# Kernel optimization log

Measured on AMD Instinct MI355X. Metric: run time of the kernel, lower is better.

## Reference

```python
import jax, jax.numpy as jnp
import numpy as np

MARGIN = 0.3
NEG_INF = jnp.float32(-1e30)


def setup_inputs() -> dict:
    key = jax.random.key(0)
    k1, k2 = jax.random.split(key)
    features = jax.random.normal(k1, (8192, 128), dtype=jnp.float32)
    labels = jax.random.randint(k2, (8192,), 0, 512)
    return {"features": features, "labels": labels}


def reference(features, labels):
    n = features.shape[0]
    # pairwise Euclidean distance, clamped like the torch code
    x2 = jnp.sum(features * features, axis=1, keepdims=True)          # [N,1]
    d2 = x2 + x2.T - 2.0 * (features @ features.T)                    # [N,N]
    dist = jnp.sqrt(jnp.clip(d2, 1e-8))

    same = labels[None, :] == labels[:, None]                          # [N,N]
    eye = jnp.eye(n, dtype=bool)
    pos_mask = same & ~eye                                             # positives, self excluded
    neg_mask = ~same

    # soft mining: softmax-weighted positive distance (weights ~ softmax(d))
    pos_logits = jnp.where(pos_mask, dist, NEG_INF)
    pw = jax.nn.softmax(pos_logits, axis=1)
    wp = jnp.sum(pw * jnp.where(pos_mask, dist, 0.0), axis=1)          # [N]

    # softmax-weighted negative distance (weights ~ softmax(-d))
    neg_logits = jnp.where(neg_mask, -dist, NEG_INF)
    nw = jax.nn.softmax(neg_logits, axis=1)
    wn = jnp.sum(nw * jnp.where(neg_mask, dist, 0.0), axis=1)          # [N]

    # soft margin: softplus(diff + margin)
    loss = jax.nn.softplus(wp - wn + MARGIN)

    # rows without any positive or any negative are skipped in the original
    valid = pos_mask.any(axis=1) & neg_mask.any(axis=1)
    loss = jnp.where(valid, loss, 0.0)
    denom = jnp.maximum(jnp.sum(valid.astype(jnp.float32)), 1.0)
    return jnp.sum(loss) / denom
```

## Files before the change

### kernel.cpp

```cpp
#include <hip/hip_runtime.h>
#include <hip/hip_bf16.h>


typedef __bf16 bf16x8 __attribute__((ext_vector_type(8)));
typedef float f32x4 __attribute__((ext_vector_type(4)));

#define NROWS 8192
#define DIM 128
#define JTILE 64
#define LDS_STRIDE 136
#define NLABELS 512
#define GCAP 64
#define MARGIN_F 0.3f
#define AK1F 2.04027892f
#define EPS_T 2.08137e-8f
#define C2F (-43.2808512f)
#define LN2F 0.69314718f

__global__ __launch_bounds__(256) void prep_kernel(const float* __restrict__ F,
                                                   const int* __restrict__ labels,
                                                   __hip_bfloat16* __restrict__ Fb,
                                                   float* __restrict__ x2,
                                                   int* __restrict__ gcnt,
                                                   int* __restrict__ gslot) {
    const int tid = threadIdx.x;
    const int wave = tid >> 6, lane = tid & 63;
    const int row = blockIdx.x * 4 + wave;
    float2 f = ((const float2*)(F + (size_t)row * DIM))[lane];
    f.x *= AK1F; f.y *= AK1F;
    ((__hip_bfloat162*)(Fb + (size_t)row * DIM))[lane] = __float22bfloat162_rn(f);
    float ss = f.x * f.x + f.y * f.y;
#pragma unroll
    for (int m = 32; m > 0; m >>= 1) ss += __shfl_xor(ss, m, 64);
    if (lane == 0) {
        x2[row] = ss;
        const int lab = labels[row];
        int pos = atomicAdd(&gcnt[lab], 1);
        if (pos < GCAP) gslot[lab * GCAP + pos] = row;
    }
}

template<bool DIAG>
__device__ __forceinline__ void tile_body(const __hip_bfloat16* __restrict__ sB,
                                          const float* __restrict__ sX2h,
                                          const bf16x8 (&a)[4],
                                          const float (&x2ih)[4],
                                          float (&nl4)[4], float (&ns4)[4],
                                          int lm, int quad, int ig0, int jbase) {
#pragma unroll
    for (int jt = 0; jt < 4; ++jt) {
        const int jl = jt * 16 + lm;
        const __hip_bfloat16* bp = sB + jl * LDS_STRIDE + quad * 8;
        const float xjh = sX2h[jl];
        f32x4 acc;
#pragma unroll
        for (int r = 0; r < 4; ++r) acc[r] = x2ih[r] + xjh;
#pragma unroll
        for (int kc = 0; kc < 4; ++kc) {
            bf16x8 b = *(const bf16x8*)(bp + kc * 32);
            acc = __builtin_amdgcn_mfma_f32_16x16x32_bf16(a[kc], b, acc, 0, 0, 0);
        }
        const int dj = jbase + jl - ig0;
#pragma unroll
        for (int r = 0; r < 4; ++r) {
            float d2h = fmaxf(-acc[r], EPS_T);
            float t = __builtin_amdgcn_sqrtf(d2h);
            float ne = __builtin_amdgcn_exp2f(-t);
            if (DIAG) ne = (dj == r) ? 0.f : ne;
            nl4[r] += ne;
            ns4[r] = fmaf(ne, t, ns4[r]);
        }
    }
}

__global__ __launch_bounds__(256, 4) void pairs_kernel(
        const __hip_bfloat16* __restrict__ Fb,
        const float* __restrict__ x2,
        const int* __restrict__ gcnt,
        const int* __restrict__ gslot,
        float2* __restrict__ partial,
        float4* __restrict__ corr,
        int jspan) {
    __shared__ __hip_bfloat16 sB[JTILE * LDS_STRIDE];
    __shared__ float sX2h[JTILE];

    const int tid = threadIdx.x;

    if (blockIdx.y < 4) {
        const int L = (int)blockIdx.y * 128 + (int)blockIdx.x;
        float* sAcc = (float*)sB;
        float* plA = sAcc;
        float* psA = sAcc + GCAP;
        float* nlA = sAcc + 2 * GCAP;
        float* nsA = sAcc + 3 * GCAP;
        const int cnt = gcnt[L];
        const int gsz = cnt < GCAP ? cnt : GCAP;
        if (gsz > 0) {
            if (tid < GCAP) { plA[tid] = 0.f; psA[tid] = 0.f; nlA[tid] = 0.f; nsA[tid] = 0.f; }
            __syncthreads();
            const int npair = gsz * gsz;
            for (int p = tid; p < npair; p += 256) {
                const int aI = p / gsz, bI = p - aI * gsz;
                if (aI != bI) {
                    const int ia = gslot[L * GCAP + aI];
                    const int ib = gslot[L * GCAP + bI];
                    const bf16x8* pa = (const bf16x8*)(Fb + (size_t)ia * DIM);
                    const bf16x8* pb = (const bf16x8*)(Fb + (size_t)ib * DIM);
                    float dot = 0.f;
#pragma unroll 4
                    for (int u = 0; u < 16; ++u) {
                        bf16x8 va = pa[u], vb = pb[u];
#pragma unroll
                        for (int e = 0; e < 8; ++e)
                            dot = fmaf((float)va[e], (float)vb[e], dot);
                    }
                    float d2h = fmaxf(0.5f * (x2[ia] + x2[ib]) - dot, EPS_T);
                    float t = __builtin_amdgcn_sqrtf(d2h);
                    float ne = __builtin_amdgcn_exp2f(-t);
                    float pe = __builtin_amdgcn_exp2f(t + C2F);
                    unsafeAtomicAdd(&nlA[aI], ne);
                    unsafeAtomicAdd(&nsA[aI], ne * t);
                    unsafeAtomicAdd(&plA[aI], pe);
                    unsafeAtomicAdd(&psA[aI], pe * t);
                }
            }
            __syncthreads();
            if (tid < gsz)
                corr[gslot[L * GCAP + tid]] =
                    make_float4(plA[tid], psA[tid], -nlA[tid], -nsA[tid]);
        }
    }

    const int wave = tid >> 6;
    const int lane = tid & 63;
    const int quad = lane >> 4;
    const int lm = lane & 15;
    const int rbase = blockIdx.x * 64 + wave * 16;

    bf16x8 a[4];
#pragma unroll
    for (int kc = 0; kc < 4; ++kc)
        a[kc] = *(const bf16x8*)(Fb + (size_t)(rbase + lm) * DIM + kc * 32 + quad * 8);

    const int ig0 = rbase + quad * 4;
    float x2ih[4];
#pragma unroll
    for (int r = 0; r < 4; ++r) x2ih[r] = -0.5f * x2[ig0 + r];

    float nl4[4] = {0,0,0,0}, ns4[4] = {0,0,0,0};

    const int j0 = blockIdx.y * jspan;
    const int jiters = jspan >> 6;
    const int djb = (int)blockIdx.x - (int)blockIdx.y * jiters;

    for (int jb = 0; jb < jiters; ++jb) {
        const int jbase = j0 + jb * JTILE;
        __syncthreads();
#pragma unroll
        for (int s = 0; s < 4; ++s) {
            int c = tid + s * 256;
            int jr = c >> 4, ck = c & 15;
            *(bf16x8*)(sB + jr * LDS_STRIDE + ck * 8) =
                *(const bf16x8*)(Fb + (size_t)(jbase + jr) * DIM + ck * 8);
        }
        if (tid < JTILE) sX2h[tid] = -0.5f * x2[jbase + tid];
        __syncthreads();

        if (jb == djb)
            tile_body<true >(sB, sX2h, a, x2ih, nl4, ns4, lm, quad, ig0, jbase);
        else
            tile_body<false>(sB, sX2h, a, x2ih, nl4, ns4, lm, quad, ig0, jbase);
    }

#pragma unroll
    for (int m = 1; m < 16; m <<= 1) {
#pragma unroll
        for (int r = 0; r < 4; ++r) {
            nl4[r] += __shfl_xor(nl4[r], m, 64);
            ns4[r] += __shfl_xor(ns4[r], m, 64);
        }
    }
    if (lm == 0) {
#pragma unroll
        for (int r = 0; r < 4; ++r)
            partial[(size_t)blockIdx.y * NROWS + ig0 + r] =
                make_float2(nl4[r], ns4[r]);
    }
}

__global__ __launch_bounds__(256) void finalize_kernel(const float2* __restrict__ partial,
                                                       const float4* __restrict__ corr,
                                                       float* __restrict__ gstat,
                                                       float* __restrict__ out,
                                                       int jsplit) {
    const int row = blockIdx.x * 256 + threadIdx.x;
    float4 c = corr[row];
    float nl = c.z, ns = c.w;
    for (int s = 0; s < jsplit; ++s) {
        float2 p = partial[(size_t)s * NROWS + row];
        nl += p.x; ns += p.y;
    }
    float sum = 0.f, cnt = 0.f;
    if (c.x > 0.f && nl > 0.f) {
        float x = fmaf(LN2F, c.y / c.x - ns / nl, MARGIN_F);
        sum = fmaxf(x, 0.f) + log1pf(__expf(-fabsf(x)));
        cnt = 1.f;
    }
#pragma unroll
    for (int m = 32; m > 0; m >>= 1) {
        sum += __shfl_xor(sum, m, 64);
        cnt += __shfl_xor(cnt, m, 64);
    }
    __shared__ float sS[4], sC[4];
    const int wave = threadIdx.x >> 6, lane = threadIdx.x & 63;
    if (lane == 0) { sS[wave] = sum; sC[wave] = cnt; }
    __syncthreads();
    if (threadIdx.x == 0) {
        unsafeAtomicAdd(&gstat[0], sS[0] + sS[1] + sS[2] + sS[3]);
        unsafeAtomicAdd(&gstat[1], sC[0] + sC[1] + sC[2] + sC[3]);
        __threadfence();
        unsigned t = atomicAdd((unsigned int*)(gstat + 2), 1u);
        if (t == (unsigned)(gridDim.x - 1)) {
            float s2 = unsafeAtomicAdd(&gstat[0], 0.f);
            float c2 = unsafeAtomicAdd(&gstat[1], 0.f);
            out[0] = s2 / fmaxf(c2, 1.f);
        }
    }
}

extern "C" void kernel_launch(void* const* d_in, const int* in_sizes, int n_in,
                              void* d_out, int out_size, void* d_ws, size_t ws_size,
                              hipStream_t stream) {
    const float* F = (const float*)d_in[0];
    const int* labels = (const int*)d_in[1];
    float* out = (float*)d_out;

    char* ws = (char*)d_ws;
    __hip_bfloat16* Fb = (__hip_bfloat16*)ws;
    size_t off = (size_t)NROWS * DIM * 2;
    float* x2 = (float*)(ws + off);   off += (size_t)NROWS * 4;
    float4* corr = (float4*)(ws + off); off += (size_t)NROWS * 16;
    int* gcnt = (int*)(ws + off);     off += (size_t)NLABELS * 4;
    float* gstat = (float*)(ws + off); off += 16;
    int* gslot = (int*)(ws + off);    off += (size_t)NLABELS * GCAP * 4;

    int jsplit = 16;
    while (jsplit > 4 && off + (size_t)jsplit * NROWS * 8 > ws_size) jsplit >>= 1;
    float2* partial = (float2*)(ws + off);

    hipMemsetAsync(gcnt, 0, (size_t)NLABELS * 4 + 16, stream);
    prep_kernel<<<NROWS / 4, 256, 0, stream>>>(F, labels, Fb, x2, gcnt, gslot);
    pairs_kernel<<<dim3(NROWS / 64, jsplit), 256, 0, stream>>>(
        Fb, x2, gcnt, gslot, partial, corr, NROWS / jsplit);
    finalize_kernel<<<NROWS / 256, 256, 0, stream>>>(partial, corr, gstat, out, jsplit);
}
```

Baseline: 115.8 us.

## Fuse prep into pairs kernel: convert fp32 to bf16 on the fly, scan labels per block

Removes the separate prep kernel and the memset. The pairs kernel now reads fp32 features directly, scales them, converts them to bf16 and computes squared norms while staging each tile in LDS. The label-group blocks find their members by scanning the labels array in LDS instead of using global atomics, and the same-label pairs are computed in fp32 from the raw features. This saves two launches and the intermediate bf16 buffer, but each of the 2048 blocks now re-converts fp32 tiles (twice the global read bytes), and 512 blocks each scan all 8192 labels.

```diff
diff --git a/kernel.cpp b/kernel.cpp
--- a/kernel.cpp
+++ b/kernel.cpp
@@ -11,38 +11,28 @@
 #define LDS_STRIDE 136
 #define NLABELS 512
 #define GCAP 64
+#define JSPLIT 16
+#define JSPAN (NROWS / JSPLIT)
+#define JITERS (JSPAN / JTILE)
 #define MARGIN_F 0.3f
 #define AK1F 2.04027892f
+#define AK1SQ 4.16273807f
 #define EPS_T 2.08137e-8f
 #define C2F (-43.2808512f)
 #define LN2F 0.69314718f
 
-__global__ __launch_bounds__(256) void prep_kernel(const float* __restrict__ F,
-                                                   const int* __restrict__ labels,
-                                                   __hip_bfloat16* __restrict__ Fb,
-                                                   float* __restrict__ x2,
-                                                   int* __restrict__ gcnt,
-                                                   int* __restrict__ gslot) {
-    const int tid = threadIdx.x;
-    const int wave = tid >> 6, lane = tid & 63;
-    const int row = blockIdx.x * 4 + wave;
-    float2 f = ((const float2*)(F + (size_t)row * DIM))[lane];
-    f.x *= AK1F; f.y *= AK1F;
-    ((__hip_bfloat162*)(Fb + (size_t)row * DIM))[lane] = __float22bfloat162_rn(f);
-    float ss = f.x * f.x + f.y * f.y;
-#pragma unroll
-    for (int m = 32; m > 0; m >>= 1) ss += __shfl_xor(ss, m, 64);
-    if (lane == 0) {
-        x2[row] = ss;
-        const int lab = labels[row];
-        int pos = atomicAdd(&gcnt[lab], 1);
-        if (pos < GCAP) gslot[lab * GCAP + pos] = row;
-    }
+__device__ __forceinline__ bf16x8 pack8(float4 f0, float4 f1) {
+    union { __hip_bfloat162 h[4]; bf16x8 v; } u;
+    u.h[0] = __float22bfloat162_rn(make_float2(f0.x, f0.y));
+    u.h[1] = __float22bfloat162_rn(make_float2(f0.z, f0.w));
+    u.h[2] = __float22bfloat162_rn(make_float2(f1.x, f1.y));
+    u.h[3] = __float22bfloat162_rn(make_float2(f1.z, f1.w));
+    return u.v;
 }
 
 template<bool DIAG>
 __device__ __forceinline__ void tile_body(const __hip_bfloat16* __restrict__ sB,
-                                          const float* __restrict__ sX2h,
+                                          const float* __restrict__ sX2,
                                           const bf16x8 (&a)[4],
                                           const float (&x2ih)[4],
                                           float (&nl4)[4], float (&ns4)[4],
@@ -51,10 +41,10 @@
     for (int jt = 0; jt < 4; ++jt) {
         const int jl = jt * 16 + lm;
         const __hip_bfloat16* bp = sB + jl * LDS_STRIDE + quad * 8;
-        const float xjh = sX2h[jl];
+        const float xj = sX2[jl];
         f32x4 acc;
 #pragma unroll
-        for (int r = 0; r < 4; ++r) acc[r] = x2ih[r] + xjh;
+        for (int r = 0; r < 4; ++r) acc[r] = fmaf(-0.5f, xj, x2ih[r]);
 #pragma unroll
         for (int kc = 0; kc < 4; ++kc) {
             bf16x8 b = *(const bf16x8*)(bp + kc * 32);
@@ -74,102 +64,132 @@
 }
 
 __global__ __launch_bounds__(256, 4) void pairs_kernel(
-        const __hip_bfloat16* __restrict__ Fb,
-        const float* __restrict__ x2,
-        const int* __restrict__ gcnt,
-        const int* __restrict__ gslot,
+        const float* __restrict__ F,
+        const int* __restrict__ labels,
         float2* __restrict__ partial,
         float4* __restrict__ corr,
-        int jspan) {
+        float* __restrict__ gstat) {
     __shared__ __hip_bfloat16 sB[JTILE * LDS_STRIDE];
-    __shared__ float sX2h[JTILE];
+    __shared__ float sX2[JTILE];
+    __shared__ int sIdx[GCAP];
+    __shared__ int sCnt;
 
     const int tid = threadIdx.x;
-
-    if (blockIdx.y < 4) {
-        const int L = (int)blockIdx.y * 128 + (int)blockIdx.x;
-        float* sAcc = (float*)sB;
-        float* plA = sAcc;
-        float* psA = sAcc + GCAP;
-        float* nlA = sAcc + 2 * GCAP;
-        float* nsA = sAcc + 3 * GCAP;
-        const int cnt = gcnt[L];
-        const int gsz = cnt < GCAP ? cnt : GCAP;
+    const int bx = blockIdx.x, by = blockIdx.y;
+
+    if (bx == 0 && by == 0 && tid < 4) gstat[tid] = 0.f;
+
+    if (by < 4) {
+        const int L = by * 128 + bx;
+        if (tid == 0) sCnt = 0;
+        __syncthreads();
+        for (int it = 0; it < NROWS / 1024; ++it) {
+            const int g = it * 1024 + tid * 4;
+            int4 lv = *(const int4*)(labels + g);
+#pragma unroll
+            for (int k = 0; k < 4; ++k) {
+                int lab = (k == 0) ? lv.x : (k == 1) ? lv.y : (k == 2) ? lv.z : lv.w;
+                if (lab == L) {
+                    int pos = atomicAdd(&sCnt, 1);
+                    if (pos < GCAP) sIdx[pos] = g + k;
+                }
+            }
+        }
+        __syncthreads();
+        const int gsz = sCnt < GCAP ? sCnt : GCAP;
         if (gsz > 0) {
+            float* sAcc = (float*)sB;
+            float* plA = sAcc;
+            float* psA = sAcc + GCAP;
+            float* nlA = sAcc + 2 * GCAP;
+            float* nsA = sAcc + 3 * GCAP;
             if (tid < GCAP) { plA[tid] = 0.f; psA[tid] = 0.f; nlA[tid] = 0.f; nsA[tid] = 0.f; }
             __syncthreads();
             const int npair = gsz * gsz;
             for (int p = tid; p < npair; p += 256) {
                 const int aI = p / gsz, bI = p - aI * gsz;
-                if (aI != bI) {
-                    const int ia = gslot[L * GCAP + aI];
-                    const int ib = gslot[L * GCAP + bI];
-                    const bf16x8* pa = (const bf16x8*)(Fb + (size_t)ia * DIM);
-                    const bf16x8* pb = (const bf16x8*)(Fb + (size_t)ib * DIM);
-                    float dot = 0.f;
-#pragma unroll 4
-                    for (int u = 0; u < 16; ++u) {
-                        bf16x8 va = pa[u], vb = pb[u];
-#pragma unroll
-                        for (int e = 0; e < 8; ++e)
-                            dot = fmaf((float)va[e], (float)vb[e], dot);
-                    }
-                    float d2h = fmaxf(0.5f * (x2[ia] + x2[ib]) - dot, EPS_T);
-                    float t = __builtin_amdgcn_sqrtf(d2h);
-                    float ne = __builtin_amdgcn_exp2f(-t);
-                    float pe = __builtin_amdgcn_exp2f(t + C2F);
-                    unsafeAtomicAdd(&nlA[aI], ne);
-                    unsafeAtomicAdd(&nsA[aI], ne * t);
-                    unsafeAtomicAdd(&plA[aI], pe);
-                    unsafeAtomicAdd(&psA[aI], pe * t);
+                if (aI == bI) continue;
+                const float4* pa = (const float4*)(F + (size_t)sIdx[aI] * DIM);
+                const float4* pb = (const float4*)(F + (size_t)sIdx[bI] * DIM);
+                float dot = 0.f, ssa = 0.f, ssb = 0.f;
+#pragma unroll 8
+                for (int u = 0; u < 32; ++u) {
+                    float4 va = pa[u], vb = pb[u];
+                    dot = fmaf(va.x, vb.x, fmaf(va.y, vb.y, fmaf(va.z, vb.z, fmaf(va.w, vb.w, dot))));
+                    ssa = fmaf(va.x, va.x, fmaf(va.y, va.y, fmaf(va.z, va.z, fmaf(va.w, va.w, ssa))));
+                    ssb = fmaf(vb.x, vb.x, fmaf(vb.y, vb.y, fmaf(vb.z, vb.z, fmaf(vb.w, vb.w, ssb))));
                 }
+                float d2h = fmaxf((0.5f * (ssa + ssb) - dot) * AK1SQ, EPS_T);
+                float t = __builtin_amdgcn_sqrtf(d2h);
+                float ne = __builtin_amdgcn_exp2f(-t);
+                float pe = __builtin_amdgcn_exp2f(t + C2F);
+                unsafeAtomicAdd(&nlA[aI], ne);
+                unsafeAtomicAdd(&nsA[aI], ne * t);
+                unsafeAtomicAdd(&plA[aI], pe);
+                unsafeAtomicAdd(&psA[aI], pe * t);
             }
             __syncthreads();
             if (tid < gsz)
-                corr[gslot[L * GCAP + tid]] =
-                    make_float4(plA[tid], psA[tid], -nlA[tid], -nsA[tid]);
-        }
+                corr[sIdx[tid]] = make_float4(plA[tid], psA[tid], -nlA[tid], -nsA[tid]);
+        }
+        __syncthreads();
     }
 
     const int wave = tid >> 6;
     const int lane = tid & 63;
     const int quad = lane >> 4;
     const int lm = lane & 15;
-    const int rbase = blockIdx.x * 64 + wave * 16;
+    const int rbase = bx * 64 + wave * 16;
 
     bf16x8 a[4];
-#pragma unroll
-    for (int kc = 0; kc < 4; ++kc)
-        a[kc] = *(const bf16x8*)(Fb + (size_t)(rbase + lm) * DIM + kc * 32 + quad * 8);
-
+    float ssq = 0.f;
+#pragma unroll
+    for (int kc = 0; kc < 4; ++kc) {
+        const float4* src = (const float4*)(F + (size_t)(rbase + lm) * DIM + kc * 32 + quad * 8);
+        float4 f0 = src[0], f1 = src[1];
+        f0.x *= AK1F; f0.y *= AK1F; f0.z *= AK1F; f0.w *= AK1F;
+        f1.x *= AK1F; f1.y *= AK1F; f1.z *= AK1F; f1.w *= AK1F;
+        ssq += f0.x*f0.x + f0.y*f0.y + f0.z*f0.z + f0.w*f0.w
+             + f1.x*f1.x + f1.y*f1.y + f1.z*f1.z + f1.w*f1.w;
+        a[kc] = pack8(f0, f1);
+    }
+    ssq += __shfl_xor(ssq, 16, 64);
+    ssq += __shfl_xor(ssq, 32, 64);
     const int ig0 = rbase + quad * 4;
     float x2ih[4];
 #pragma unroll
-    for (int r = 0; r < 4; ++r) x2ih[r] = -0.5f * x2[ig0 + r];
+    for (int r = 0; r < 4; ++r)
+        x2ih[r] = -0.5f * __shfl(ssq, quad * 4 + r, 64);
 
     float nl4[4] = {0,0,0,0}, ns4[4] = {0,0,0,0};
-
-    const int j0 = blockIdx.y * jspan;
-    const int jiters = jspan >> 6;
-    const int djb = (int)blockIdx.x - (int)blockIdx.y * jiters;
-
-    for (int jb = 0; jb < jiters; ++jb) {
+    const int j0 = by * JSPAN;
+    const int djb = bx - by * JITERS;
+
+    for (int jb = 0; jb < JITERS; ++jb) {
         const int jbase = j0 + jb * JTILE;
         __syncthreads();
 #pragma unroll
-        for (int s = 0; s < 4; ++s) {
-            int c = tid + s * 256;
-            int jr = c >> 4, ck = c & 15;
-            *(bf16x8*)(sB + jr * LDS_STRIDE + ck * 8) =
-                *(const bf16x8*)(Fb + (size_t)(jbase + jr) * DIM + ck * 8);
-        }
-        if (tid < JTILE) sX2h[tid] = -0.5f * x2[jbase + tid];
+        for (int u = 0; u < 8; ++u) {
+            const int c = u * 256 + tid;
+            const int jr = c >> 5;
+            const int ck = c & 31;
+            float4 f = ((const float4*)F)[(size_t)(jbase + jr) * 32 + ck];
+            f.x *= AK1F; f.y *= AK1F; f.z *= AK1F; f.w *= AK1F;
+            float s4 = f.x*f.x + f.y*f.y + f.z*f.z + f.w*f.w;
+#pragma unroll
+            for (int m = 1; m <= 16; m <<= 1) s4 += __shfl_xor(s4, m, 64);
+            if ((tid & 31) == 0) sX2[jr] = s4;
+            union { __hip_bfloat162 h[2]; uint2 u2; } cv;
+            cv.h[0] = __float22bfloat162_rn(make_float2(f.x, f.y));
+            cv.h[1] = __float22bfloat162_rn(make_float2(f.z, f.w));
+            *(uint2*)(sB + jr * LDS_STRIDE + ck * 4) = cv.u2;
+        }
         __syncthreads();
 
         if (jb == djb)
-            tile_body<true >(sB, sX2h, a, x2ih, nl4, ns4, lm, quad, ig0, jbase);
+            tile_body<true >(sB, sX2, a, x2ih, nl4, ns4, lm, quad, ig0, jbase);
         else
-            tile_body<false>(sB, sX2h, a, x2ih, nl4, ns4, lm, quad, ig0, jbase);
+            tile_body<false>(sB, sX2, a, x2ih, nl4, ns4, lm, quad, ig0, jbase);
     }
 
 #pragma unroll
@@ -183,20 +203,19 @@
     if (lm == 0) {
 #pragma unroll
         for (int r = 0; r < 4; ++r)
-            partial[(size_t)blockIdx.y * NROWS + ig0 + r] =
-                make_float2(nl4[r], ns4[r]);
+            partial[(size_t)by * NROWS + ig0 + r] = make_float2(nl4[r], ns4[r]);
     }
 }
 
 __global__ __launch_bounds__(256) void finalize_kernel(const float2* __restrict__ partial,
                                                        const float4* __restrict__ corr,
                                                        float* __restrict__ gstat,
-                                                       float* __restrict__ out,
-                                                       int jsplit) {
+                                                       float* __restrict__ out) {
     const int row = blockIdx.x * 256 + threadIdx.x;
     float4 c = corr[row];
     float nl = c.z, ns = c.w;
-    for (int s = 0; s < jsplit; ++s) {
+#pragma unroll
+    for (int s = 0; s < JSPLIT; ++s) {
         float2 p = partial[(size_t)s * NROWS + row];
         nl += p.x; ns += p.y;
     }
@@ -219,7 +238,7 @@
         unsafeAtomicAdd(&gstat[0], sS[0] + sS[1] + sS[2] + sS[3]);
         unsafeAtomicAdd(&gstat[1], sC[0] + sC[1] + sC[2] + sC[3]);
         __threadfence();
-        unsigned t = atomicAdd((unsigned int*)(gstat + 2), 1u);
+        unsigned t = atomicAdd((unsigned*)(gstat + 2), 1u);
         if (t == (unsigned)(gridDim.x - 1)) {
             float s2 = unsafeAtomicAdd(&gstat[0], 0.f);
             float c2 = unsafeAtomicAdd(&gstat[1], 0.f);
@@ -236,21 +255,13 @@
     float* out = (float*)d_out;
 
     char* ws = (char*)d_ws;
-    __hip_bfloat16* Fb = (__hip_bfloat16*)ws;
-    size_t off = (size_t)NROWS * DIM * 2;
-    float* x2 = (float*)(ws + off);   off += (size_t)NROWS * 4;
-    float4* corr = (float4*)(ws + off); off += (size_t)NROWS * 16;
-    int* gcnt = (int*)(ws + off);     off += (size_t)NLABELS * 4;
-    float* gstat = (float*)(ws + off); off += 16;
-    int* gslot = (int*)(ws + off);    off += (size_t)NLABELS * GCAP * 4;
-
-    int jsplit = 16;
-    while (jsplit > 4 && off + (size_t)jsplit * NROWS * 8 > ws_size) jsplit >>= 1;
+    float4* corr = (float4*)ws;
+    size_t off = (size_t)NROWS * 16;
     float2* partial = (float2*)(ws + off);
-
-    hipMemsetAsync(gcnt, 0, (size_t)NLABELS * 4 + 16, stream);
-    prep_kernel<<<NROWS / 4, 256, 0, stream>>>(F, labels, Fb, x2, gcnt, gslot);
-    pairs_kernel<<<dim3(NROWS / 64, jsplit), 256, 0, stream>>>(
-        Fb, x2, gcnt, gslot, partial, corr, NROWS / jsplit);
-    finalize_kernel<<<NROWS / 256, 256, 0, stream>>>(partial, corr, gstat, out, jsplit);
-}
+    off += (size_t)JSPLIT * NROWS * 8;
+    float* gstat = (float*)(ws + off);
+
+    pairs_kernel<<<dim3(NROWS / 64, JSPLIT), 256, 0, stream>>>(
+        F, labels, partial, corr, gstat);
+    finalize_kernel<<<NROWS / 256, 256, 0, stream>>>(partial, corr, gstat, out);
+}
```

Result: slower. 154.5 us (+33.4%).
